# Optimization experiments

Hardware: AMD Instinct MI355X
Metric: run time of the kernel (lower is better)

Reference implementation:

```python
import jax, jax.numpy as jnp
import numpy as np

N, E, D = 50000, 800000, 128
CLAMP = 2.0  # coord_weights_clamp_value


def setup_inputs() -> dict:
    key = jax.random.key(0)
    ks = jax.random.split(key, 12)
    rn = lambda k, shape, scale: jax.random.normal(k, shape, jnp.float32) * scale
    s = lambda fan_in: 1.0 / np.sqrt(fan_in)
    h = rn(ks[0], (N, D), 1.0)
    x = rn(ks[1], (N, 3), 1.0)
    edges = jax.random.randint(ks[2], (2, E), 0, N)
    # edge MLP: Linear(2D+1 -> D), SiLU, Linear(D -> D), SiLU
    we1 = rn(ks[3], (2 * D + 1, D), s(2 * D + 1)); be1 = jnp.zeros((D,), jnp.float32)
    we2 = rn(ks[4], (D, D), s(D));                 be2 = jnp.zeros((D,), jnp.float32)
    # node MLP: Linear(2D -> D), SiLU, Linear(D -> D)
    wn1 = rn(ks[5], (2 * D, D), s(2 * D));         bn1 = jnp.zeros((D,), jnp.float32)
    wn2 = rn(ks[6], (D, D), s(D));                 bn2 = jnp.zeros((D,), jnp.float32)
    # coord MLP: Linear(D -> D), SiLU, Linear(D -> 1, no bias, small init)
    wc1 = rn(ks[7], (D, D), s(D));                 bc1 = jnp.zeros((D,), jnp.float32)
    wc2 = rn(ks[8], (D, 1), 0.001)
    return dict(h=h, x=x, edges=edges, we1=we1, be1=be1, we2=we2, be2=be2,
                wn1=wn1, bn1=bn1, wn2=wn2, bn2=bn2, wc1=wc1, bc1=bc1, wc2=wc2)


def reference(h, x, edges, we1, be1, we2, be2, wn1, bn1, wn2, bn2, wc1, bc1, wc2):
    n = h.shape[0]
    row, col = edges[0], edges[1]
    # coord2radial
    coord_diff = x[row] - x[col]                                  # [E, 3]
    radial = jnp.sum(coord_diff * coord_diff, axis=1, keepdims=True)  # [E, 1]
    # edge model: phi_e(h_i, h_j, ||x_i - x_j||^2)
    e_in = jnp.concatenate([h[row], h[col], radial], axis=1)      # [E, 2D+1]
    m = jax.nn.silu(jax.nn.silu(e_in @ we1 + be1) @ we2 + be2)    # [E, D]
    # coord model: x_i += mean_j (x_i - x_j) * phi_x(m_ij), clamped
    w = jax.nn.silu(m @ wc1 + bc1) @ wc2                          # [E, 1]
    trans = jnp.clip(coord_diff * w, -CLAMP, CLAMP)               # [E, 3]
    ones = jnp.ones((row.shape[0], 1), m.dtype)
    cnt = jax.ops.segment_sum(ones, row, num_segments=n)          # [N, 1]
    agg_x = jax.ops.segment_sum(trans, row, num_segments=n) / jnp.maximum(cnt, 1.0)
    x_out = x + agg_x
    # node model: h_i += phi_h(h_i, sum_j m_ij)  (residual=True)
    agg_m = jax.ops.segment_sum(m, row, num_segments=n)           # [N, D]
    h_up = jax.nn.silu(jnp.concatenate([h, agg_m], axis=1) @ wn1 + bn1) @ wn2 + bn2
    h_out = h + h_up
    return (h_out, x_out)
```

## Files before the change

### kernel.cpp

```cpp
#include <hip/hip_runtime.h>
#include <hip/hip_bf16.h>
#include <stdint.h>

typedef unsigned short u16;
typedef __bf16 bf16x8 __attribute__((ext_vector_type(8)));
typedef float f32x4 __attribute__((ext_vector_type(4)));

#define DD 128

__device__ __forceinline__ u16 f2bf(float f) {
  uint32_t r;
  asm("v_cvt_pk_bf16_f32 %0, %1, %2" : "=v"(r) : "v"(f), "v"(f));
  return (u16)r;
}
__device__ __forceinline__ float bf2f(u16 h) {
  union { uint32_t u; float f; } v; v.u = ((uint32_t)h) << 16;
  return v.f;
}
__device__ __forceinline__ uint32_t pack2(float a, float b) {
  uint32_t r;
  asm("v_cvt_pk_bf16_f32 %0, %1, %2" : "=v"(r) : "v"(a), "v"(b));
  return r;
}
__device__ __forceinline__ float silu_(float v) {
  return v * __builtin_amdgcn_rcpf(1.0f + __expf(-v));
}
__device__ __forceinline__ f32x4 MFMA(bf16x8 a, bf16x8 b, f32x4 c) {
  return __builtin_amdgcn_mfma_f32_16x16x32_bf16(a, b, c, 0, 0, 0);
}
#define LGKM_FENCE() do { asm volatile("s_waitcnt lgkmcnt(0)" ::: "memory"); __builtin_amdgcn_sched_barrier(0); } while (0)

__global__ __launch_bounds__(256) void kprep(
    const float* __restrict__ we1, const float* __restrict__ we2,
    const float* __restrict__ wn1, const float* __restrict__ wn2,
    const float* __restrict__ wc1, u16* __restrict__ frags) {
  const int total = 16384 * 5 + 32768;
  for (int idx = blockIdx.x * blockDim.x + threadIdx.x; idx < total;
       idx += gridDim.x * blockDim.x) {
    const float* src; int segbase;
    if (idx < 16384)      { src = we1;          segbase = 0; }
    else if (idx < 32768) { src = we1 + 16384;  segbase = 16384; }
    else if (idx < 49152) { src = we2;          segbase = 32768; }
    else if (idx < 65536) { src = wc1;          segbase = 49152; }
    else if (idx < 81920) { src = wn2;          segbase = 65536; }
    else                  { src = wn1;          segbase = 81920; }
    int local = idx - segbase;
    int k = local >> 7, n = local & 127;
    float v = src[k * 128 + n];
    int s = k >> 5, i = k & 7, g = (k >> 3) & 3;
    int lane = (g << 4) | (n & 15), f = n >> 4;
    frags[segbase + (((s * 8 + f) * 64 + lane) << 3) + i] = f2bf(v);
  }
}

__global__ __launch_bounds__(256) void kpq(
    const float* __restrict__ h, const float* __restrict__ be1,
    const u16* __restrict__ wA, const u16* __restrict__ wB,
    u16* __restrict__ Pb, u16* __restrict__ Qb, int N) {
  __shared__ u16 act[64 * 128];
  const int tid = threadIdx.x;
  const int w = tid >> 6, l = tid & 63;
  const int lm = l & 15, lh = l >> 4;
  const int base = blockIdx.x * 64;

  {
    const int q = l & 3;
    const int rowL = w * 16 + (l >> 2);
    int node = base + rowL; if (node >= N) node = N - 1;
    const float* hs = h + (size_t)node * 128 + q * 32;
    #pragma unroll
    for (int c4 = 0; c4 < 4; ++c4) {
      float4 v0 = *(const float4*)(hs + c4 * 8);
      float4 v1 = *(const float4*)(hs + c4 * 8 + 4);
      uint4 pk;
      pk.x = pack2(v0.x, v0.y); pk.y = pack2(v0.z, v0.w);
      pk.z = pack2(v1.x, v1.y); pk.w = pack2(v1.z, v1.w);
      int c = q * 4 + c4;
      *(uint4*)&act[rowL * 128 + (((c ^ (rowL & 7))) << 3)] = pk;
    }
  }
  LGKM_FENCE();
  const int rowA = w * 16 + lm, sw = rowA & 7;
  bf16x8 a[4];
  #pragma unroll
  for (int s = 0; s < 4; ++s)
    a[s] = *(const bf16x8*)&act[rowA * 128 + (((4 * s + lh) ^ sw) << 3)];
  float be1r[8];
  #pragma unroll
  for (int f = 0; f < 8; ++f) be1r[f] = be1[16 * f + lm];

  f32x4 acc[8] = {};
  #pragma unroll
  for (int s = 0; s < 4; ++s)
    #pragma unroll
    for (int f = 0; f < 8; ++f)
      acc[f] = MFMA(a[s], *(const bf16x8*)(wA + (((s * 8 + f) * 64 + l) << 3)), acc[f]);
  #pragma unroll
  for (int f = 0; f < 8; ++f)
    #pragma unroll
    for (int r = 0; r < 4; ++r) {
      int row = base + w * 16 + lh * 4 + r;
      Pb[(size_t)row * 128 + 16 * f + lm] = f2bf(acc[f][r] + be1r[f]);
    }

  f32x4 acc2[8] = {};
  #pragma unroll
  for (int s = 0; s < 4; ++s)
    #pragma unroll
    for (int f = 0; f < 8; ++f)
      acc2[f] = MFMA(a[s], *(const bf16x8*)(wB + (((s * 8 + f) * 64 + l) << 3)), acc2[f]);
  #pragma unroll
  for (int f = 0; f < 8; ++f)
    #pragma unroll
    for (int r = 0; r < 4; ++r) {
      int row = base + w * 16 + lh * 4 + r;
      Qb[(size_t)row * 128 + 16 * f + lm] = f2bf(acc2[f][r]);
    }
}

__global__ __launch_bounds__(256) void kedge(
    const float* __restrict__ x, const int* __restrict__ edges,
    const float* __restrict__ we1, const float* __restrict__ be2,
    const float* __restrict__ bc1, const float* __restrict__ wc2,
    const u16* __restrict__ Pb, const u16* __restrict__ Qb,
    const u16* __restrict__ we2f, const u16* __restrict__ wc1f,
    float* __restrict__ aggm, float* __restrict__ aggx, int E) {
  __shared__ u16 act[64 * 128];
  __shared__ float w1c[128];
  const int tid = threadIdx.x;
  if (tid < 128) w1c[tid] = we1[256 * 128 + tid];
  __syncthreads();

  const int w = tid >> 6, l = tid & 63;
  const int lm = l & 15, lh = l >> 4;
  float be2r[8], bc1r[8], wc2r[8];
  #pragma unroll
  for (int f = 0; f < 8; ++f) {
    be2r[f] = be2[16 * f + lm];
    bc1r[f] = bc1[16 * f + lm];
    wc2r[f] = wc2[16 * f + lm];
  }

  const int tb = blockIdx.x * 64 + w * 16;
  int eMine = tb + lm;
  int eC = eMine < E ? eMine : E - 1;
  const int rowv = edges[eC];
  const int colv = edges[E + eC];
  float cdx = x[rowv * 3]     - x[colv * 3];
  float cdy = x[rowv * 3 + 1] - x[colv * 3 + 1];
  float cdz = x[rowv * 3 + 2] - x[colv * 3 + 2];
  float radial = cdx * cdx + cdy * cdy + cdz * cdz;

  {
    const int el = l >> 2, q = l & 3;
    int rG = __shfl(rowv, el), cG = __shfl(colv, el);
    float rad = __shfl(radial, el);
    const int rowL = w * 16 + el;
    const u16* Pp = Pb + (size_t)rG * 128 + q * 32;
    const u16* Qp = Qb + (size_t)cG * 128 + q * 32;
    #pragma unroll
    for (int c4 = 0; c4 < 4; ++c4) {
      uint4 pv = *(const uint4*)(Pp + c4 * 8);
      uint4 qv = *(const uint4*)(Qp + c4 * 8);
      uint32_t pw[4] = {pv.x, pv.y, pv.z, pv.w};
      uint32_t qw[4] = {qv.x, qv.y, qv.z, qv.w};
      uint32_t ow[4];
      #pragma unroll
      for (int jj = 0; jj < 4; ++jj) {
        int fb = q * 32 + c4 * 8 + jj * 2;
        float t0 = bf2f((u16)(pw[jj] & 0xffff)) + bf2f((u16)(qw[jj] & 0xffff)) + rad * w1c[fb];
        float t1 = bf2f((u16)(pw[jj] >> 16))    + bf2f((u16)(qw[jj] >> 16))    + rad * w1c[fb + 1];
        ow[jj] = pack2(silu_(t0), silu_(t1));
      }
      int c = q * 4 + c4;
      *(uint4*)&act[rowL * 128 + ((c ^ (rowL & 7)) << 3)] =
          make_uint4(ow[0], ow[1], ow[2], ow[3]);
    }
  }
  LGKM_FENCE();

  const int rowA = w * 16 + lm, sw = rowA & 7;
  bf16x8 a[4];
  #pragma unroll
  for (int s = 0; s < 4; ++s)
    a[s] = *(const bf16x8*)&act[rowA * 128 + (((4 * s + lh) ^ sw) << 3)];

  f32x4 acc[8] = {};
  #pragma unroll
  for (int s = 0; s < 4; ++s)
    #pragma unroll
    for (int f = 0; f < 8; ++f)
      acc[f] = MFMA(a[s], *(const bf16x8*)(we2f + (((s * 8 + f) * 64 + l) << 3)), acc[f]);

  #pragma unroll
  for (int f = 0; f < 8; ++f)
    #pragma unroll
    for (int r = 0; r < 4; ++r) {
      float m = silu_(acc[f][r] + be2r[f]);
      int row = w * 16 + lh * 4 + r, col = 16 * f + lm;
      act[row * 128 + (((col >> 3) ^ (row & 7)) << 3) + (col & 7)] = f2bf(m);
    }
  LGKM_FENCE();

  bf16x8 a2[4];
  #pragma unroll
  for (int s = 0; s < 4; ++s)
    a2[s] = *(const bf16x8*)&act[rowA * 128 + (((4 * s + lh) ^ sw) << 3)];
  f32x4 acc3[8] = {};
  #pragma unroll
  for (int s = 0; s < 4; ++s)
    #pragma unroll
    for (int f = 0; f < 8; ++f)
      acc3[f] = MFMA(a2[s], *(const bf16x8*)(wc1f + (((s * 8 + f) * 64 + l) << 3)), acc3[f]);

  float wp[4] = {0.f, 0.f, 0.f, 0.f};
  #pragma unroll
  for (int f = 0; f < 8; ++f)
    #pragma unroll
    for (int r = 0; r < 4; ++r)
      wp[r] += silu_(acc3[f][r] + bc1r[f]) * wc2r[f];
  #pragma unroll
  for (int r = 0; r < 4; ++r) {
    wp[r] += __shfl_xor(wp[r], 1);
    wp[r] += __shfl_xor(wp[r], 2);
    wp[r] += __shfl_xor(wp[r], 4);
    wp[r] += __shfl_xor(wp[r], 8);
  }
  int er[4]; bool vr[4];
  float cdxr[4], cdyr[4], cdzr[4];
  #pragma unroll
  for (int r = 0; r < 4; ++r) {
    er[r] = __shfl(rowv, lh * 4 + r);
    vr[r] = (tb + lh * 4 + r) < E;
    cdxr[r] = __shfl(cdx, lh * 4 + r);
    cdyr[r] = __shfl(cdy, lh * 4 + r);
    cdzr[r] = __shfl(cdz, lh * 4 + r);
  }

  if (lm < 4) {
    #pragma unroll
    for (int r = 0; r < 4; ++r) {
      if (vr[r]) {
        float wv = wp[r];
        float v3;
        if (lm == 0)      v3 = fminf(fmaxf(cdxr[r] * wv, -2.0f), 2.0f);
        else if (lm == 1) v3 = fminf(fmaxf(cdyr[r] * wv, -2.0f), 2.0f);
        else if (lm == 2) v3 = fminf(fmaxf(cdzr[r] * wv, -2.0f), 2.0f);
        else              v3 = 1.0f;
        unsafeAtomicAdd(&aggx[(size_t)er[r] * 4 + lm], v3);
      }
    }
  }

  #pragma unroll
  for (int f = 0; f < 8; ++f)
    #pragma unroll
    for (int r = 0; r < 4; ++r) {
      if (vr[r]) {
        float m = silu_(acc[f][r] + be2r[f]);
        unsafeAtomicAdd(&aggm[(size_t)er[r] * 128 + 16 * f + lm], m);
      }
    }
}

__global__ __launch_bounds__(256) void knode(
    const float* __restrict__ h, const float* __restrict__ x,
    const float* __restrict__ aggm, const float* __restrict__ aggx,
    const float* __restrict__ bn1, const float* __restrict__ bn2,
    const u16* __restrict__ wn1f, const u16* __restrict__ wn2f,
    float* __restrict__ out, int N) {
  __shared__ u16 act[64 * 256];
  __shared__ u16 act2[64 * 128];
  const int tid = threadIdx.x;
  const int w = tid >> 6, l = tid & 63;
  const int lm = l & 15, lh = l >> 4;
  const int base = blockIdx.x * 64;

  if (tid < 192) {
    int n = base + tid / 3, c = tid - (tid / 3) * 3;
    if (n < N) {
      float ct = fmaxf(aggx[(size_t)n * 4 + 3], 1.0f);
      out[(size_t)N * 128 + (size_t)n * 3 + c] =
          x[(size_t)n * 3 + c] + aggx[(size_t)n * 4 + c] / ct;
    }
  }

  {
    const int q = l & 3;
    const int rowL = w * 16 + (l >> 2);
    int node = base + rowL; if (node >= N) node = N - 1;
    const float* src = (q < 2) ? (h + (size_t)node * 128 + q * 64)
                               : (aggm + (size_t)node * 128 + (q - 2) * 64);
    #pragma unroll
    for (int c8 = 0; c8 < 8; ++c8) {
      float4 v0 = *(const float4*)(src + c8 * 8);
      float4 v1 = *(const float4*)(src + c8 * 8 + 4);
      uint4 pk;
      pk.x = pack2(v0.x, v0.y); pk.y = pack2(v0.z, v0.w);
      pk.z = pack2(v1.x, v1.y); pk.w = pack2(v1.z, v1.w);
      int c = q * 8 + c8;
      *(uint4*)&act[rowL * 256 + ((c ^ (rowL & 7)) << 3)] = pk;
    }
  }
  LGKM_FENCE();

  const int rowA = w * 16 + lm, sw = rowA & 7;
  float bn1r[8], bn2r[8];
  #pragma unroll
  for (int f = 0; f < 8; ++f) {
    bn1r[f] = bn1[16 * f + lm];
    bn2r[f] = bn2[16 * f + lm];
  }
  bf16x8 a[8];
  #pragma unroll
  for (int s = 0; s < 8; ++s)
    a[s] = *(const bf16x8*)&act[rowA * 256 + (((4 * s + lh) ^ sw) << 3)];
  f32x4 acc[8] = {};
  #pragma unroll
  for (int s = 0; s < 8; ++s)
    #pragma unroll
    for (int f = 0; f < 8; ++f)
      acc[f] = MFMA(a[s], *(const bf16x8*)(wn1f + (((s * 8 + f) * 64 + l) << 3)), acc[f]);
  #pragma unroll
  for (int f = 0; f < 8; ++f)
    #pragma unroll
    for (int r = 0; r < 4; ++r) {
      int row = w * 16 + lh * 4 + r, col = 16 * f + lm;
      act2[row * 128 + (((col >> 3) ^ (row & 7)) << 3) + (col & 7)] =
          f2bf(silu_(acc[f][r] + bn1r[f]));
    }
  LGKM_FENCE();

  bf16x8 a2[4];
  #pragma unroll
  for (int s = 0; s < 4; ++s)
    a2[s] = *(const bf16x8*)&act2[rowA * 128 + (((4 * s + lh) ^ sw) << 3)];
  f32x4 acc2[8] = {};
  #pragma unroll
  for (int s = 0; s < 4; ++s)
    #pragma unroll
    for (int f = 0; f < 8; ++f)
      acc2[f] = MFMA(a2[s], *(const bf16x8*)(wn2f + (((s * 8 + f) * 64 + l) << 3)), acc2[f]);
  #pragma unroll
  for (int f = 0; f < 8; ++f)
    #pragma unroll
    for (int r = 0; r < 4; ++r) {
      int n2 = base + w * 16 + lh * 4 + r;
      if (n2 < N) {
        int col = 16 * f + lm;
        out[(size_t)n2 * 128 + col] =
            h[(size_t)n2 * 128 + col] + acc2[f][r] + bn2r[f];
      }
    }
}

extern "C" void kernel_launch(void* const* d_in, const int* in_sizes, int n_in,
                              void* d_out, int out_size, void* d_ws, size_t ws_size,
                              hipStream_t stream) {
  const float* h   = (const float*)d_in[0];
  const float* x   = (const float*)d_in[1];
  const int* edges = (const int*)d_in[2];
  const float* we1 = (const float*)d_in[3];
  const float* be1 = (const float*)d_in[4];
  const float* we2 = (const float*)d_in[5];
  const float* be2 = (const float*)d_in[6];
  const float* wn1 = (const float*)d_in[7];
  const float* bn1 = (const float*)d_in[8];
  const float* wn2 = (const float*)d_in[9];
  const float* bn2 = (const float*)d_in[10];
  const float* wc1 = (const float*)d_in[11];
  const float* bc1 = (const float*)d_in[12];
  const float* wc2 = (const float*)d_in[13];

  const int N = in_sizes[0] / DD;
  const int E = in_sizes[2] / 2;
  const int NT = (N + 63) & ~63;

  u16* Pb    = (u16*)d_ws;
  u16* Qb    = Pb + (size_t)NT * DD;
  u16* frags = Qb + (size_t)NT * DD;
  float* aggm = (float*)(frags + 114688);
  float* aggx = aggm + (size_t)NT * DD;
  size_t need = (size_t)NT * DD * 2 * 2 + 114688 * 2 +
                (size_t)NT * (DD * 4 + 16);
  if (ws_size < need) return;

  hipMemsetAsync(aggm, 0, (size_t)NT * (DD * 4 + 16), stream);
  hipLaunchKernelGGL(kprep, dim3(64), dim3(256), 0, stream,
                     we1, we2, wn1, wn2, wc1, frags);
  hipLaunchKernelGGL(kpq, dim3(NT / 64), dim3(256), 0, stream,
                     h, be1, frags, frags + 16384, Pb, Qb, N);
  hipLaunchKernelGGL(kedge, dim3((E + 63) / 64), dim3(256), 0, stream,
                     x, edges, we1, be2, bc1, wc2, Pb, Qb,
                     frags + 32768, frags + 49152, aggm, aggx, E);
  hipLaunchKernelGGL(knode, dim3(NT / 64), dim3(256), 0, stream,
                     h, x, aggm, aggx, bn1, bn2,
                     frags + 81920, frags + 65536, (float*)d_out, N);
}
```

Baseline: 453.8 us.

## Split edge kernel into MLP compute pass and separate atomic scatter pass

The fused edge kernel is split in two when the workspace is large enough. kedgeA runs the edge and coord MLPs and writes the per-edge message m (bf16, in a tile-transposed layout) plus the clamped coordinate deltas and the row index to global buffers. A new kscat kernel then reads those buffers and does the atomic adds into aggm and aggx. The goal is to take the atomic scatter traffic off the MFMA-heavy kernel, at the cost of an extra round trip of an E×128 bf16 buffer through memory. Messages are also now rounded to bf16 before aggregation, which slightly reduces precision.

```diff
diff --git a/kernel.cpp b/kernel.cpp
--- a/kernel.cpp
+++ b/kernel.cpp
@@ -118,13 +118,14 @@
     }
 }
 
-__global__ __launch_bounds__(256) void kedge(
+
+__global__ __launch_bounds__(256) void kedgeA(
     const float* __restrict__ x, const int* __restrict__ edges,
     const float* __restrict__ we1, const float* __restrict__ be2,
     const float* __restrict__ bc1, const float* __restrict__ wc2,
     const u16* __restrict__ Pb, const u16* __restrict__ Qb,
     const u16* __restrict__ we2f, const u16* __restrict__ wc1f,
-    float* __restrict__ aggm, float* __restrict__ aggx, int E) {
+    u16* __restrict__ mT, float* __restrict__ trans4, int E) {
   __shared__ u16 act[64 * 128];
   __shared__ float w1c[128];
   const int tid = threadIdx.x;
@@ -192,6 +193,175 @@
     for (int f = 0; f < 8; ++f)
       acc[f] = MFMA(a[s], *(const bf16x8*)(we2f + (((s * 8 + f) * 64 + l) << 3)), acc[f]);
 
+  bool ev[4];
+  #pragma unroll
+  for (int r = 0; r < 4; ++r) ev[r] = (tb + lh * 4 + r) < E;
+  u16* mTb = mT + (size_t)(blockIdx.x * 4 + w) * 2048;
+
+  #pragma unroll
+  for (int f = 0; f < 8; ++f)
+    #pragma unroll
+    for (int r = 0; r < 4; ++r) {
+      float m = silu_(acc[f][r] + be2r[f]);
+      u16 mv = f2bf(m);
+      int row = w * 16 + lh * 4 + r, col = 16 * f + lm;
+      act[row * 128 + (((col >> 3) ^ (row & 7)) << 3) + (col & 7)] = mv;
+      if (ev[r]) mTb[((lh * 4 + r) * 16 + lm) * 8 + f] = mv;
+    }
+  LGKM_FENCE();
+
+  bf16x8 a2[4];
+  #pragma unroll
+  for (int s = 0; s < 4; ++s)
+    a2[s] = *(const bf16x8*)&act[rowA * 128 + (((4 * s + lh) ^ sw) << 3)];
+  f32x4 acc3[8] = {};
+  #pragma unroll
+  for (int s = 0; s < 4; ++s)
+    #pragma unroll
+    for (int f = 0; f < 8; ++f)
+      acc3[f] = MFMA(a2[s], *(const bf16x8*)(wc1f + (((s * 8 + f) * 64 + l) << 3)), acc3[f]);
+
+  float wp[4] = {0.f, 0.f, 0.f, 0.f};
+  #pragma unroll
+  for (int f = 0; f < 8; ++f)
+    #pragma unroll
+    for (int r = 0; r < 4; ++r)
+      wp[r] += silu_(acc3[f][r] + bc1r[f]) * wc2r[f];
+  #pragma unroll
+  for (int r = 0; r < 4; ++r) {
+    wp[r] += __shfl_xor(wp[r], 1);
+    wp[r] += __shfl_xor(wp[r], 2);
+    wp[r] += __shfl_xor(wp[r], 4);
+    wp[r] += __shfl_xor(wp[r], 8);
+  }
+  #pragma unroll
+  for (int r = 0; r < 4; ++r) {
+    int erv = __shfl(rowv, lh * 4 + r);
+    float cdxr = __shfl(cdx, lh * 4 + r);
+    float cdyr = __shfl(cdy, lh * 4 + r);
+    float cdzr = __shfl(cdz, lh * 4 + r);
+    if (lm < 4 && ev[r]) {
+      float wv = wp[r];
+      float v3;
+      if (lm == 0)      v3 = fminf(fmaxf(cdxr * wv, -2.0f), 2.0f);
+      else if (lm == 1) v3 = fminf(fmaxf(cdyr * wv, -2.0f), 2.0f);
+      else if (lm == 2) v3 = fminf(fmaxf(cdzr * wv, -2.0f), 2.0f);
+      else              v3 = __int_as_float(erv);
+      trans4[(size_t)(tb + lh * 4 + r) * 4 + lm] = v3;
+    }
+  }
+}
+
+__global__ __launch_bounds__(256) void kscat(
+    const u16* __restrict__ mT, const float* __restrict__ trans4,
+    float* __restrict__ aggm, float* __restrict__ aggx, int E) {
+  const int tid = threadIdx.x;
+  const int w = tid >> 6, l = tid & 63;
+  const int lh = l >> 4, lm = l & 15;
+  const int tile = blockIdx.x * 4 + w;
+  const int tb = tile * 16;
+
+  const u16* base = mT + (size_t)tile * 2048;
+  bf16x8 ch[4];
+  #pragma unroll
+  for (int r = 0; r < 4; ++r)
+    ch[r] = *(const bf16x8*)(base + ((lh * 4 + r) * 16 + lm) * 8);
+
+  int eL = tb + (l >> 2);
+  float tv = (eL < E) ? trans4[(size_t)eL * 4 + (l & 3)] : __int_as_float(-1);
+
+  int erOwn = __float_as_int(__shfl(tv, (l >> 2) * 4 + 3));
+  if (erOwn >= 0) {
+    float val = ((l & 3) == 3) ? 1.0f : tv;
+    unsafeAtomicAdd(&aggx[(size_t)erOwn * 4 + (l & 3)], val);
+  }
+
+  #pragma unroll
+  for (int r = 0; r < 4; ++r) {
+    int er = __float_as_int(__shfl(tv, (lh * 4 + r) * 4 + 3));
+    if (er >= 0) {
+      const u16* hp = (const u16*)&ch[r];
+      #pragma unroll
+      for (int f = 0; f < 8; ++f)
+        unsafeAtomicAdd(&aggm[(size_t)er * 128 + 16 * f + lm], bf2f(hp[f]));
+    }
+  }
+}
+
+__global__ __launch_bounds__(256) void kedge_mono(
+    const float* __restrict__ x, const int* __restrict__ edges,
+    const float* __restrict__ we1, const float* __restrict__ be2,
+    const float* __restrict__ bc1, const float* __restrict__ wc2,
+    const u16* __restrict__ Pb, const u16* __restrict__ Qb,
+    const u16* __restrict__ we2f, const u16* __restrict__ wc1f,
+    float* __restrict__ aggm, float* __restrict__ aggx, int E) {
+  __shared__ u16 act[64 * 128];
+  __shared__ float w1c[128];
+  const int tid = threadIdx.x;
+  if (tid < 128) w1c[tid] = we1[256 * 128 + tid];
+  __syncthreads();
+
+  const int w = tid >> 6, l = tid & 63;
+  const int lm = l & 15, lh = l >> 4;
+  float be2r[8], bc1r[8], wc2r[8];
+  #pragma unroll
+  for (int f = 0; f < 8; ++f) {
+    be2r[f] = be2[16 * f + lm];
+    bc1r[f] = bc1[16 * f + lm];
+    wc2r[f] = wc2[16 * f + lm];
+  }
+
+  const int tb = blockIdx.x * 64 + w * 16;
+  int eMine = tb + lm;
+  int eC = eMine < E ? eMine : E - 1;
+  const int rowv = edges[eC];
+  const int colv = edges[E + eC];
+  float cdx = x[rowv * 3]     - x[colv * 3];
+  float cdy = x[rowv * 3 + 1] - x[colv * 3 + 1];
+  float cdz = x[rowv * 3 + 2] - x[colv * 3 + 2];
+  float radial = cdx * cdx + cdy * cdy + cdz * cdz;
+
+  {
+    const int el = l >> 2, q = l & 3;
+    int rG = __shfl(rowv, el), cG = __shfl(colv, el);
+    float rad = __shfl(radial, el);
+    const int rowL = w * 16 + el;
+    const u16* Pp = Pb + (size_t)rG * 128 + q * 32;
+    const u16* Qp = Qb + (size_t)cG * 128 + q * 32;
+    #pragma unroll
+    for (int c4 = 0; c4 < 4; ++c4) {
+      uint4 pv = *(const uint4*)(Pp + c4 * 8);
+      uint4 qv = *(const uint4*)(Qp + c4 * 8);
+      uint32_t pw[4] = {pv.x, pv.y, pv.z, pv.w};
+      uint32_t qw[4] = {qv.x, qv.y, qv.z, qv.w};
+      uint32_t ow[4];
+      #pragma unroll
+      for (int jj = 0; jj < 4; ++jj) {
+        int fb = q * 32 + c4 * 8 + jj * 2;
+        float t0 = bf2f((u16)(pw[jj] & 0xffff)) + bf2f((u16)(qw[jj] & 0xffff)) + rad * w1c[fb];
+        float t1 = bf2f((u16)(pw[jj] >> 16))    + bf2f((u16)(qw[jj] >> 16))    + rad * w1c[fb + 1];
+        ow[jj] = pack2(silu_(t0), silu_(t1));
+      }
+      int c = q * 4 + c4;
+      *(uint4*)&act[rowL * 128 + ((c ^ (rowL & 7)) << 3)] =
+          make_uint4(ow[0], ow[1], ow[2], ow[3]);
+    }
+  }
+  LGKM_FENCE();
+
+  const int rowA = w * 16 + lm, sw = rowA & 7;
+  bf16x8 a[4];
+  #pragma unroll
+  for (int s = 0; s < 4; ++s)
+    a[s] = *(const bf16x8*)&act[rowA * 128 + (((4 * s + lh) ^ sw) << 3)];
+
+  f32x4 acc[8] = {};
+  #pragma unroll
+  for (int s = 0; s < 4; ++s)
+    #pragma unroll
+    for (int f = 0; f < 8; ++f)
+      acc[f] = MFMA(a[s], *(const bf16x8*)(we2f + (((s * 8 + f) * 64 + l) << 3)), acc[f]);
+
   #pragma unroll
   for (int f = 0; f < 8; ++f)
     #pragma unroll
@@ -251,7 +421,6 @@
       }
     }
   }
-
   #pragma unroll
   for (int f = 0; f < 8; ++f)
     #pragma unroll
@@ -375,24 +544,37 @@
   const int N = in_sizes[0] / DD;
   const int E = in_sizes[2] / 2;
   const int NT = (N + 63) & ~63;
+  const int ET = (E + 15) & ~15;
 
   u16* Pb    = (u16*)d_ws;
   u16* Qb    = Pb + (size_t)NT * DD;
   u16* frags = Qb + (size_t)NT * DD;
   float* aggm = (float*)(frags + 114688);
   float* aggx = aggm + (size_t)NT * DD;
-  size_t need = (size_t)NT * DD * 2 * 2 + 114688 * 2 +
-                (size_t)NT * (DD * 4 + 16);
-  if (ws_size < need) return;
+  u16* mT     = (u16*)(aggx + (size_t)NT * 4);
+  float* trans4 = (float*)(mT + (size_t)ET * DD);
+
+  size_t need_small = (size_t)NT * DD * 2 * 2 + 114688 * 2 +
+                      (size_t)NT * (DD * 4 + 16);
+  size_t need_big = need_small + (size_t)ET * DD * 2 + (size_t)ET * 16;
+  if (ws_size < need_small) return;
 
   hipMemsetAsync(aggm, 0, (size_t)NT * (DD * 4 + 16), stream);
   hipLaunchKernelGGL(kprep, dim3(64), dim3(256), 0, stream,
                      we1, we2, wn1, wn2, wc1, frags);
   hipLaunchKernelGGL(kpq, dim3(NT / 64), dim3(256), 0, stream,
                      h, be1, frags, frags + 16384, Pb, Qb, N);
-  hipLaunchKernelGGL(kedge, dim3((E + 63) / 64), dim3(256), 0, stream,
-                     x, edges, we1, be2, bc1, wc2, Pb, Qb,
-                     frags + 32768, frags + 49152, aggm, aggx, E);
+  if (ws_size >= need_big) {
+    hipLaunchKernelGGL(kedgeA, dim3((E + 63) / 64), dim3(256), 0, stream,
+                       x, edges, we1, be2, bc1, wc2, Pb, Qb,
+                       frags + 32768, frags + 49152, mT, trans4, E);
+    hipLaunchKernelGGL(kscat, dim3((ET / 16 + 3) / 4), dim3(256), 0, stream,
+                       mT, trans4, aggm, aggx, E);
+  } else {
+    hipLaunchKernelGGL(kedge_mono, dim3((E + 63) / 64), dim3(256), 0, stream,
+                       x, edges, we1, be2, bc1, wc2, Pb, Qb,
+                       frags + 32768, frags + 49152, aggm, aggx, E);
+  }
   hipLaunchKernelGGL(knode, dim3(NT / 64), dim3(256), 0, stream,
                      h, x, aggm, aggx, bn1, bn2,
                      frags + 81920, frags + 65536, (float*)d_out, N);
```

After: 453.9 us. Within noise of the previous version (+0.0%).
